# Optimization experiments

Measured on AMD Instinct MI355X. Metric: run time of the kernel, lower is better.

## Reference

```python
import jax, jax.numpy as jnp
import numpy as np

M, K, N = 1024, 8192, 8192
PACK = 16  # 16 two-bit codes per int32 word


def _pack_ternary(codes):
    # codes: (N, K) int32 with values in {0,1,3} -> (N, K//16) int32
    c = codes.reshape(N, K // PACK, PACK).astype(jnp.uint32)
    shifts = (jnp.arange(PACK, dtype=jnp.uint32) * 2)
    packed = jnp.sum(c << shifts, axis=-1, dtype=jnp.uint32)
    return jax.lax.bitcast_convert_type(packed, jnp.int32)


def setup_inputs() -> dict:
    key = jax.random.key(0)
    kx, kw, kb = jax.random.split(key, 3)
    x = jax.random.normal(kx, (M, K), dtype=jnp.float16)
    # ternary codes drawn from {0,1,3} (code 2 is unused by the format)
    vals = jnp.array([0, 1, 3], dtype=jnp.int32)
    codes = vals[jax.random.randint(kw, (N, K), 0, 3)]
    packed_w = _pack_ternary(codes)
    bias = jax.random.normal(kb, (N,), dtype=jnp.float16)
    return {"x": x, "packed_w": packed_w, "bias": bias}


def _unpack(packed_w):
    # (N, K//16) int32 -> (N, K) fp16 weights with values in {0,1,3}
    shifts = jnp.arange(PACK, dtype=jnp.int32) * 2
    w = (packed_w[:, :, None] >> shifts) & 3  # mask keeps low 2 bits even with arithmetic shift
    return w.reshape(packed_w.shape[0], -1).astype(jnp.float16)


def reference(x, packed_w, bias):
    w = _unpack(packed_w)  # (N, K)
    # Y = X W^T + b, fp32 accumulation as in the CUDA/Triton GEMM, fp16 output
    y = jnp.einsum('mk,nk->mn', x, w, preferred_element_type=jnp.float32)
    y = y.astype(jnp.float16) + bias
    return y
```

## Files before the change

kernel.cpp:

```cpp
#include <hip/hip_runtime.h>
#include <hip/hip_fp16.h>
#include <stdint.h>

#define M_DIM 1024
#define N_DIM 8192
#define K_DIM 8192
#define KP    (K_DIM / 16)

#define BM 128
#define BN 128
#define BK 64
#define NTHREADS 256
#define B_STRIDE 144

#define MT_STRIDE 2097152
#define KT_STRIDE 16384

typedef _Float16 half8   __attribute__((ext_vector_type(8)));
typedef __fp16   fp16x2  __attribute__((ext_vector_type(2)));
typedef float    f32x4   __attribute__((ext_vector_type(4)));
typedef float    f32x16  __attribute__((ext_vector_type(16)));

__device__ __forceinline__ uint32_t cvt2(float a, float b) {
  fp16x2 p = __builtin_amdgcn_cvt_pkrtz(a, b);
  return __builtin_bit_cast(uint32_t, p);
}

__device__ __forceinline__ half8 dec_frag(uint32_t word, uint32_t sh) {
  const uint32_t T = 0x42063C00u;
  uint32_t h  = (word >> sh) & 0xFFFFu;
  uint32_t W  = (h & 0x3333u) | ((h << 14) & 0x33330000u);
  uint32_t c0 = __builtin_amdgcn_perm(0u, W, 0x04040200u);
  uint32_t c1 = __builtin_amdgcn_perm(0u, W, 0x04040301u);
  uint32_t s0 = (c0 * 0x1001u) & 0x03030303u;
  uint32_t s1 = (c1 * 0x1001u) & 0x03030303u;
  uint32_t P0 = __builtin_amdgcn_perm(0u, T, s0);
  uint32_t P1 = __builtin_amdgcn_perm(0u, T, s1);
  uint4 v;
  v.x = __builtin_amdgcn_perm(P0, 0u, 0x05000400u);
  v.y = __builtin_amdgcn_perm(P0, 0u, 0x07000600u);
  v.z = __builtin_amdgcn_perm(P1, 0u, 0x05000400u);
  v.w = __builtin_amdgcn_perm(P1, 0u, 0x07000600u);
  return __builtin_bit_cast(half8, v);
}

__global__ __launch_bounds__(256)
void cvt_x_t(const float* __restrict__ x, char* __restrict__ xhT) {
  __shared__ __align__(16) char st[16384];
  const int b  = blockIdx.x;
  const int mt = b >> 7, kt = b & 127;
  const int t  = threadIdx.x;
#pragma unroll
  for (int p = 0; p < 8; ++p) {
    int f   = t + 256 * p;
    int R   = f >> 4;
    int cc4 = f & 15;
    float4 v = *(const float4*)(x + (size_t)(mt * 128 + R) * K_DIM + kt * 64 + cc4 * 4);
    uint32_t w0 = cvt2(v.x, v.y), w1 = cvt2(v.z, v.w);
    int c8 = cc4 >> 1, hh = cc4 & 1;
    int i32 = R >> 5, r = R & 31, ks = c8 >> 1, q = c8 & 1;
    *(uint2*)(st + i32 * 4096 + ks * 1024 + q * 512 + r * 16 + hh * 8) = make_uint2(w0, w1);
  }
  __syncthreads();
  char* outb = xhT + (size_t)mt * MT_STRIDE + (size_t)kt * KT_STRIDE;
#pragma unroll
  for (int e = 0; e < 4; ++e) {
    int d = (e * 256 + t) * 16;
    *(uint4*)(outb + d) = *(const uint4*)(st + d);
  }
}

__global__ __launch_bounds__(NTHREADS, 2)
void ternary_gemm_dc(const char* __restrict__ xhT,
                     const int*  __restrict__ pw,
                     const float* __restrict__ bias,
                     float*       __restrict__ out) {
  __shared__ __align__(16) char stg[2 * 2048];

  const int tid  = threadIdx.x;
  const int lane = tid & 63;
  const int w    = tid >> 6;
  const int wm   = w >> 1, wn = w & 1;
  const int bid  = blockIdx.x;
  const int mt   = bid & 7;
  const int bm   = mt * BM;
  const int bn   = (bid >> 3) * BN;

  const char* pA[2];
#pragma unroll
  for (int i = 0; i < 2; ++i)
    pA[i] = xhT + (size_t)mt * MT_STRIDE + (wm * 2 + i) * 4096 + lane * 16;

  const int rT = tid >> 1, hT = tid & 1;
  const int2* gB = (const int2*)pw + (size_t)(bn + rT) * (KP / 2) + hT;
  const int stOff = rT * 16 + hT * 8;

  int rowOff[2];
#pragma unroll
  for (int j = 0; j < 2; ++j)
    rowOff[j] = (wn * 64 + j * 32 + (lane & 31)) * 16;
  const uint32_t sh = (lane >> 5) * 16;

  f32x16 acc[2][2];
#pragma unroll
  for (int i = 0; i < 2; ++i)
#pragma unroll
    for (int j = 0; j < 2; ++j) acc[i][j] = (f32x16)(0.f);

  const int NT = K_DIM / BK;

  *(int2*)(stg + stOff) = gB[0];
  half8 aA[2][4], aB[2][4];
#pragma unroll
  for (int i = 0; i < 2; ++i)
#pragma unroll
    for (int ks = 0; ks < 4; ++ks)
      aA[i][ks] = *(const half8*)(pA[i] + ks * 1024);
#pragma unroll
  for (int i = 0; i < 2; ++i) pA[i] += KT_STRIDE;
  int2 wcur = gB[2];
  __syncthreads();

  auto step = [&](half8 (&aC)[2][4], half8 (&aN)[2][4], int cur, int kt) {
#pragma unroll
    for (int i = 0; i < 2; ++i)
#pragma unroll
      for (int ks = 0; ks < 4; ++ks)
        aN[i][ks] = *(const half8*)(pA[i] + ks * 1024);
    if (kt < NT - 2) {
#pragma unroll
      for (int i = 0; i < 2; ++i) pA[i] += KT_STRIDE;
    }
    int kn2 = (kt + 2 < NT) ? (kt + 2) : (NT - 1);
    int2 wnxt = gB[kn2 * 2];

    uint32_t wr0[4], wr1[4];
    *(uint4*)wr0 = *(const uint4*)(stg + cur * 2048 + rowOff[0]);
    *(uint4*)wr1 = *(const uint4*)(stg + cur * 2048 + rowOff[1]);
    *(int2*)(stg + (cur ^ 1) * 2048 + stOff) = wcur;

#pragma unroll
    for (int ks = 0; ks < 4; ++ks) {
      half8 bf0 = dec_frag(wr0[ks], sh);
      half8 bf1 = dec_frag(wr1[ks], sh);
      acc[0][0] = __builtin_amdgcn_mfma_f32_32x32x16_f16(aC[0][ks], bf0, acc[0][0], 0, 0, 0);
      acc[0][1] = __builtin_amdgcn_mfma_f32_32x32x16_f16(aC[0][ks], bf1, acc[0][1], 0, 0, 0);
      acc[1][0] = __builtin_amdgcn_mfma_f32_32x32x16_f16(aC[1][ks], bf0, acc[1][0], 0, 0, 0);
      acc[1][1] = __builtin_amdgcn_mfma_f32_32x32x16_f16(aC[1][ks], bf1, acc[1][1], 0, 0, 0);
    }

    __syncthreads();
    wcur = wnxt;
  };

  for (int kt = 0; kt < NT; kt += 2) {
    step(aA, aB, 0, kt);
    step(aB, aA, 1, kt + 1);
  }

#pragma unroll
  for (int j = 0; j < 2; ++j) {
    int n = bn + wn * 64 + j * 32 + (lane & 31);
    __half hb = __float2half_rn(bias[n]);
#pragma unroll
    for (int i = 0; i < 2; ++i) {
      int mbase = bm + wm * 64 + i * 32 + 4 * (lane >> 5);
#pragma unroll
      for (int reg = 0; reg < 16; ++reg) {
        int m = mbase + (reg & 3) + 8 * (reg >> 2);
        __half hy = __float2half_rn(acc[i][j][reg]);
        out[(size_t)m * N_DIM + n] = __half2float(__hadd(hy, hb));
      }
    }
  }
}

__device__ __forceinline__ uint32_t unpack_pair16(uint32_t u, int p) {
  uint32_t c0 = (u >> (4 * p)) & 3u;
  uint32_t c1 = (u >> (4 * p + 2)) & 3u;
  uint32_t lo = (c0 & 1u) * 0x3C00u + (c0 >> 1) * 0x0600u;
  uint32_t hi = (c1 & 1u) * 0x3C00u + (c1 >> 1) * 0x0600u;
  return lo | (hi << 16);
}

__global__ __launch_bounds__(NTHREADS, 2)
void ternary_gemm(const float* __restrict__ x,
                  const int*   __restrict__ pw,
                  const float* __restrict__ bias,
                  float*       __restrict__ out) {
  __shared__ __align__(16) char AsB[128 * B_STRIDE];
  __shared__ __align__(16) char BsB[128 * B_STRIDE];

  const int tid  = threadIdx.x;
  const int lane = tid & 63;
  const int w    = tid >> 6;
  const int wm   = w >> 1, wn = w & 1;
  const int bid  = blockIdx.x;
  const int bm   = (bid & 7) * 128;
  const int bn   = (bid >> 3) * 128;

  const int rT = tid >> 1, hT = tid & 1;
  const float* gA = x + (size_t)(bm + rT) * K_DIM + hT * 32;
  char* const  lA = AsB + rT * B_STRIDE + hT * 64;
  const int2* gB = (const int2*)pw + (size_t)(bn + rT) * (KP / 2) + hT;
  char* dBp[4];
#pragma unroll
  for (int h = 0; h < 4; ++h)
    dBp[h] = BsB + rT * B_STRIDE + (hT * 4 + h) * 16;

  int offA[4][2], offB[4][2];
#pragma unroll
  for (int i = 0; i < 4; ++i)
#pragma unroll
    for (int ks = 0; ks < 2; ++ks) {
      int c = ks * 4 + (lane >> 4);
      offA[i][ks] = (wm * 64 + i * 16 + (lane & 15)) * B_STRIDE + c * 16;
      offB[i][ks] = (wn * 64 + i * 16 + (lane & 15)) * B_STRIDE + c * 16;
    }

  f32x4 acc[4][4];
#pragma unroll
  for (int i = 0; i < 4; ++i)
#pragma unroll
    for (int j = 0; j < 4; ++j)
      acc[i][j] = (f32x4){0.f, 0.f, 0.f, 0.f};

  const int NT = K_DIM / BK;
  for (int kt = 0; kt < NT; ++kt) {
    __syncthreads();
    int2 wcur = gB[kt * 2];
    float4 av[8];
#pragma unroll
    for (int v = 0; v < 8; ++v) av[v] = *(const float4*)(gA + kt * BK + v * 4);
    uint32_t d0[8], d1[8];
#pragma unroll
    for (int p = 0; p < 8; ++p) d0[p] = unpack_pair16((uint32_t)wcur.x, p);
#pragma unroll
    for (int p = 0; p < 8; ++p) d1[p] = unpack_pair16((uint32_t)wcur.y, p);
    *(uint4*)dBp[0] = make_uint4(d0[0], d0[1], d0[2], d0[3]);
    *(uint4*)dBp[1] = make_uint4(d0[4], d0[5], d0[6], d0[7]);
    *(uint4*)dBp[2] = make_uint4(d1[0], d1[1], d1[2], d1[3]);
    *(uint4*)dBp[3] = make_uint4(d1[4], d1[5], d1[6], d1[7]);
#pragma unroll
    for (int v = 0; v < 4; ++v) {
      uint4 aw;
      aw.x = cvt2(av[2 * v].x, av[2 * v].y);
      aw.y = cvt2(av[2 * v].z, av[2 * v].w);
      aw.z = cvt2(av[2 * v + 1].x, av[2 * v + 1].y);
      aw.w = cvt2(av[2 * v + 1].z, av[2 * v + 1].w);
      *(uint4*)(lA + v * 16) = aw;
    }
    __syncthreads();
#pragma unroll
    for (int ks = 0; ks < 2; ++ks) {
      half8 af[4], bf[4];
#pragma unroll
      for (int i = 0; i < 4; ++i) af[i] = *(const half8*)(AsB + offA[i][ks]);
#pragma unroll
      for (int j = 0; j < 4; ++j) bf[j] = *(const half8*)(BsB + offB[j][ks]);
#pragma unroll
      for (int i = 0; i < 4; ++i)
#pragma unroll
        for (int j = 0; j < 4; ++j)
          acc[i][j] = __builtin_amdgcn_mfma_f32_16x16x32_f16(af[i], bf[j], acc[i][j], 0, 0, 0);
    }
  }
#pragma unroll
  for (int j = 0; j < 4; ++j) {
    int n = bn + wn * 64 + j * 16 + (lane & 15);
    __half hb = __float2half_rn(bias[n]);
#pragma unroll
    for (int i = 0; i < 4; ++i) {
      int m0 = bm + wm * 64 + i * 16 + (lane >> 4) * 4;
#pragma unroll
      for (int r = 0; r < 4; ++r) {
        __half hy = __float2half_rn(acc[i][j][r]);
        out[(size_t)(m0 + r) * N_DIM + n] = __half2float(__hadd(hy, hb));
      }
    }
  }
}

extern "C" void kernel_launch(void* const* d_in, const int* in_sizes, int n_in,
                              void* d_out, int out_size, void* d_ws, size_t ws_size,
                              hipStream_t stream) {
  (void)in_sizes; (void)n_in; (void)out_size;
  const float* x    = (const float*)d_in[0];
  const int*   pwp  = (const int*)d_in[1];
  const float* bias = (const float*)d_in[2];
  float*       outp = (float*)d_out;

  const size_t need = (size_t)M_DIM * K_DIM * 2;
  if (ws_size >= need) {
    char* xhT = (char*)d_ws;
    cvt_x_t<<<8 * 128, 256, 0, stream>>>(x, xhT);
    dim3 grid((M_DIM / BM) * (N_DIM / BN));
    ternary_gemm_dc<<<grid, NTHREADS, 0, stream>>>(xhT, pwp, bias, outp);
  } else {
    dim3 grid((M_DIM / 128) * (N_DIM / 128));
    ternary_gemm<<<grid, NTHREADS, 0, stream>>>(x, pwp, bias, outp);
  }
}
```

Measured before the change: 234.0 us.

## Stage A tiles through LDS with global_load_lds double buffering

The X (A operand) tiles are now copied from global memory straight into double-buffered LDS with global_load_lds. Waves sharing the same M rows then read their fragments from LDS, where before each wave loaded them from global memory into registers. This removes the duplicated global A loads across the two N-waves and frees the registers that held prefetched A fragments. The cost is 32KB of extra LDS, LDS read traffic inside the MFMA loop, and a dependence on the barrier ordering the asynchronous LDS writes correctly.

```diff
diff --git a/kernel.cpp b/kernel.cpp
--- a/kernel.cpp
+++ b/kernel.cpp
@@ -24,6 +24,12 @@
 __device__ __forceinline__ uint32_t cvt2(float a, float b) {
   fp16x2 p = __builtin_amdgcn_cvt_pkrtz(a, b);
   return __builtin_bit_cast(uint32_t, p);
+}
+
+__device__ __forceinline__ void gload_lds16(const char* g, char* l) {
+  __builtin_amdgcn_global_load_lds(
+      (const __attribute__((address_space(1))) void*)g,
+      (__attribute__((address_space(3))) void*)l, 16, 0, 0);
 }
 
 __device__ __forceinline__ half8 dec_frag(uint32_t word, uint32_t sh) {
@@ -75,6 +81,7 @@
                      const int*  __restrict__ pw,
                      const float* __restrict__ bias,
                      float*       __restrict__ out) {
+  __shared__ __align__(16) char Ast[2 * 16384];
   __shared__ __align__(16) char stg[2 * 2048];
 
   const int tid  = threadIdx.x;
@@ -86,10 +93,9 @@
   const int bm   = mt * BM;
   const int bn   = (bid >> 3) * BN;
 
-  const char* pA[2];
-#pragma unroll
-  for (int i = 0; i < 2; ++i)
-    pA[i] = xhT + (size_t)mt * MT_STRIDE + (wm * 2 + i) * 4096 + lane * 16;
+  const char* gAs = xhT + (size_t)mt * MT_STRIDE + w * 4096 + lane * 16;
+  char* const lA0 = Ast + w * 4096;
+  char* const lA1 = Ast + 16384 + w * 4096;
 
   const int rT = tid >> 1, hT = tid & 1;
   const int2* gB = (const int2*)pw + (size_t)(bn + rT) * (KP / 2) + hT;
@@ -101,6 +107,8 @@
     rowOff[j] = (wn * 64 + j * 32 + (lane & 31)) * 16;
   const uint32_t sh = (lane >> 5) * 16;
 
+  const char* const aPtr = Ast + wm * 8192 + lane * 16;
+
   f32x16 acc[2][2];
 #pragma unroll
   for (int i = 0; i < 2; ++i)
@@ -109,44 +117,38 @@
 
   const int NT = K_DIM / BK;
 
+  auto stageA = [&](char* lbase, int kt) {
+    const char* g = gAs + (size_t)kt * KT_STRIDE;
+#pragma unroll
+    for (int e = 0; e < 4; ++e)
+      gload_lds16(g + e * 1024, lbase + e * 1024);
+  };
+
+  stageA(lA0, 0);
   *(int2*)(stg + stOff) = gB[0];
-  half8 aA[2][4], aB[2][4];
-#pragma unroll
-  for (int i = 0; i < 2; ++i)
-#pragma unroll
-    for (int ks = 0; ks < 4; ++ks)
-      aA[i][ks] = *(const half8*)(pA[i] + ks * 1024);
-#pragma unroll
-  for (int i = 0; i < 2; ++i) pA[i] += KT_STRIDE;
   int2 wcur = gB[2];
   __syncthreads();
 
-  auto step = [&](half8 (&aC)[2][4], half8 (&aN)[2][4], int cur, int kt) {
-#pragma unroll
-    for (int i = 0; i < 2; ++i)
-#pragma unroll
-      for (int ks = 0; ks < 4; ++ks)
-        aN[i][ks] = *(const half8*)(pA[i] + ks * 1024);
-    if (kt < NT - 2) {
-#pragma unroll
-      for (int i = 0; i < 2; ++i) pA[i] += KT_STRIDE;
-    }
-    int kn2 = (kt + 2 < NT) ? (kt + 2) : (NT - 1);
-    int2 wnxt = gB[kn2 * 2];
+  auto step = [&](int cur, int kt) {
+    if (kt + 1 < NT) stageA(cur ? lA0 : lA1, kt + 1);
 
     uint32_t wr0[4], wr1[4];
     *(uint4*)wr0 = *(const uint4*)(stg + cur * 2048 + rowOff[0]);
     *(uint4*)wr1 = *(const uint4*)(stg + cur * 2048 + rowOff[1]);
     *(int2*)(stg + (cur ^ 1) * 2048 + stOff) = wcur;
+    int kn2 = (kt + 2 < NT) ? (kt + 2) : (NT - 1);
+    int2 wnxt = gB[kn2 * 2];
 
 #pragma unroll
     for (int ks = 0; ks < 4; ++ks) {
+      half8 a0 = *(const half8*)(aPtr + cur * 16384 + 0 * 4096 + ks * 1024);
+      half8 a1 = *(const half8*)(aPtr + cur * 16384 + 1 * 4096 + ks * 1024);
       half8 bf0 = dec_frag(wr0[ks], sh);
       half8 bf1 = dec_frag(wr1[ks], sh);
-      acc[0][0] = __builtin_amdgcn_mfma_f32_32x32x16_f16(aC[0][ks], bf0, acc[0][0], 0, 0, 0);
-      acc[0][1] = __builtin_amdgcn_mfma_f32_32x32x16_f16(aC[0][ks], bf1, acc[0][1], 0, 0, 0);
-      acc[1][0] = __builtin_amdgcn_mfma_f32_32x32x16_f16(aC[1][ks], bf0, acc[1][0], 0, 0, 0);
-      acc[1][1] = __builtin_amdgcn_mfma_f32_32x32x16_f16(aC[1][ks], bf1, acc[1][1], 0, 0, 0);
+      acc[0][0] = __builtin_amdgcn_mfma_f32_32x32x16_f16(a0, bf0, acc[0][0], 0, 0, 0);
+      acc[0][1] = __builtin_amdgcn_mfma_f32_32x32x16_f16(a0, bf1, acc[0][1], 0, 0, 0);
+      acc[1][0] = __builtin_amdgcn_mfma_f32_32x32x16_f16(a1, bf0, acc[1][0], 0, 0, 0);
+      acc[1][1] = __builtin_amdgcn_mfma_f32_32x32x16_f16(a1, bf1, acc[1][1], 0, 0, 0);
     }
 
     __syncthreads();
@@ -154,8 +156,8 @@
   };
 
   for (int kt = 0; kt < NT; kt += 2) {
-    step(aA, aB, 0, kt);
-    step(aB, aA, 1, kt + 1);
+    step(0, kt);
+    step(1, kt + 1);
   }
 
 #pragma unroll
```

Result: slower. 240.5 us (+2.8%).
